# Performance work log

Hardware: AMD Instinct MI355X
Metric: run time of the kernel (lower is better)

## Reference

```python
import jax, jax.numpy as jnp
import numpy as np

D_MODEL = 1024
NUM_HEADS = 16
D_K = D_MODEL // NUM_HEADS


def setup_inputs() -> dict:
    key = jax.random.key(0)
    ks = jax.random.split(key, 7)
    B, S = 4, 2048
    lim = float(np.sqrt(6.0 / (D_MODEL + D_MODEL)))  # xavier uniform
    x = jax.random.normal(ks[0], (B, S, D_MODEL), dtype=jnp.float32)
    w_q = jax.random.uniform(ks[1], (D_MODEL, D_MODEL), jnp.float32, -lim, lim)
    w_k = jax.random.uniform(ks[2], (D_MODEL, D_MODEL), jnp.float32, -lim, lim)
    w_v = jax.random.uniform(ks[3], (D_MODEL, D_MODEL), jnp.float32, -lim, lim)
    w_o = jax.random.uniform(ks[4], (D_MODEL, D_MODEL), jnp.float32, -lim, lim)
    b_o = jnp.zeros((D_MODEL,), jnp.float32)
    ln_g = jnp.ones((D_MODEL,), jnp.float32)
    ln_b = jnp.zeros((D_MODEL,), jnp.float32)
    return {"x": x, "w_q": w_q, "w_k": w_k, "w_v": w_v, "w_o": w_o,
            "b_o": b_o, "ln_g": ln_g, "ln_b": ln_b}


def _layer_norm(y, g, b, eps=1e-5):
    mu = jnp.mean(y, axis=-1, keepdims=True)
    var = jnp.var(y, axis=-1, keepdims=True)
    return (y - mu) * jax.lax.rsqrt(var + eps) * g + b


def reference(x, w_q, w_k, w_v, w_o, b_o, ln_g, ln_b):
    B, S, D = x.shape
    # Linear weights stored torch-style [out, in]: y = x @ W^T
    def proj(w):
        return jnp.einsum('bsd,ed->bse', x, w).reshape(B, S, NUM_HEADS, D_K).transpose(0, 2, 1, 3)
    Q, K, V = proj(w_q), proj(w_k), proj(w_v)  # [B, H, S, d_k]
    scores = jnp.einsum('bhqd,bhkd->bhqk', Q, K) / jnp.sqrt(jnp.float32(D_K))
    attn = jax.nn.softmax(scores, axis=-1)  # dropout identity at eval
    out = jnp.einsum('bhqk,bhkd->bhqd', attn, V)  # [B, H, S, d_k]
    out = out.transpose(0, 2, 1, 3).reshape(B, S, D)
    out = jnp.einsum('bsd,ed->bse', out, w_o) + b_o
    return _layer_norm(x + out, ln_g, ln_b)
```

## Files before the change

kernel.cpp:

```cpp
#include <hip/hip_runtime.h>

typedef __bf16 bf16;
typedef bf16 v8bf __attribute__((ext_vector_type(8)));
typedef bf16 v4bf __attribute__((ext_vector_type(4)));
typedef float v4f __attribute__((ext_vector_type(4)));
typedef float v16f __attribute__((ext_vector_type(16)));
typedef unsigned int u32;
typedef u32 v4u __attribute__((ext_vector_type(4)));

#define GAS __attribute__((address_space(1)))
#define LAS __attribute__((address_space(3)))

constexpr int D    = 1024;
constexpr int ROWS = 8192;

__global__ __launch_bounds__(256) void cast_all(
    const float* __restrict__ x,
    const float* __restrict__ wq, const float* __restrict__ wk,
    const float* __restrict__ wv, const float* __restrict__ wo,
    bf16* __restrict__ xb, bf16* __restrict__ wqb, bf16* __restrict__ wkb,
    bf16* __restrict__ wvb, bf16* __restrict__ wob)
{
    int i = blockIdx.x * 256 + threadIdx.x;
    const float* src; bf16* dst; int off;
    if (i < 2 * 1024 * 1024) { src = x; dst = xb; off = i; }
    else {
        int j = i - 2 * 1024 * 1024;
        int w = j >> 18;
        off = j & ((1 << 18) - 1);
        src = (w == 0) ? wq : (w == 1) ? wk : (w == 2) ? wv : wo;
        dst = (w == 0) ? wqb : (w == 1) ? wkb : (w == 2) ? wvb : wob;
    }
    float4 v = ((const float4*)src)[off];
    v4bf o;
    o[0] = (bf16)v.x; o[1] = (bf16)v.y; o[2] = (bf16)v.z; o[3] = (bf16)v.w;
    ((v4bf*)dst)[off] = o;
}

template<int MODE, int NTN>
__global__ __launch_bounds__(512, 2) void gemm8(
    const bf16* __restrict__ A, const bf16* __restrict__ W,
    bf16* __restrict__ Oq, bf16* __restrict__ Ok, bf16* __restrict__ Ov,
    float* __restrict__ Of, const float* __restrict__ bias,
    const float* __restrict__ X)
{
    __shared__ bf16 Abuf[3][256 * 64];
    __shared__ bf16 Bbuf[3][128 * 64];

    const int id   = blockIdx.x;
    const int wgid = (id & 7) * (4 * NTN) + (id >> 3);
    const int mT   = wgid / NTN;
    const int nT   = wgid - mT * NTN;
    const long rowA0 = (long)mT * 256;
    const long colB0 = (long)nT * 128;

    const int tid  = threadIdx.x;
    const int lane = tid & 63;
    const int wave = tid >> 6;
    const int quad = lane >> 4;
    const int l16  = lane & 15;
    const int wm   = (wave >> 1) * 64;
    const int wn   = (wave & 1) * 64;

    const int srow = wave * 8 + (lane >> 3);
    const int scol = ((lane & 7) ^ (lane >> 3)) * 8;
    const bf16* gA = A + (rowA0 + srow) * D + scol;
    const bf16* gB = W + (colB0 + srow) * D + scol;
    const int dstOff = wave * 512;

    const v4f vzero = {0.f, 0.f, 0.f, 0.f};
    v4f acc[4][4];
    #pragma unroll
    for (int i = 0; i < 4; i++)
        #pragma unroll
        for (int j = 0; j < 4; j++) acc[i][j] = vzero;

    int sa[2], sb[2];
    #pragma unroll
    for (int ks = 0; ks < 2; ks++) {
        const int ch = ((ks * 4 + quad) ^ (l16 & 7)) * 8;
        sa[ks] = (wm + l16) * 64 + ch;
        sb[ks] = (wn + l16) * 64 + ch;
    }

    auto stage_full = [&](int bi, int t) {
        const bf16* a = gA + (long)t * 64;
        const bf16* b = gB + (long)t * 64;
        #pragma unroll
        for (int i = 0; i < 4; i++)
            __builtin_amdgcn_global_load_lds(
                (const GAS void*)(a + (long)i * 64 * D),
                (LAS void*)(&Abuf[bi][i * 4096 + dstOff]), 16, 0, 0);
        #pragma unroll
        for (int i = 0; i < 2; i++)
            __builtin_amdgcn_global_load_lds(
                (const GAS void*)(b + (long)i * 64 * D),
                (LAS void*)(&Bbuf[bi][i * 4096 + dstOff]), 16, 0, 0);
    };

    constexpr int NT = 16;
    stage_full(0, 0);
    stage_full(1, 1);
    asm volatile("s_waitcnt vmcnt(6)" ::: "memory");
    __builtin_amdgcn_s_barrier();

    for (int t = 0; t < NT; ++t) {
        const int bi = t % 3;
        const int bs = (t + 2) % 3;
        const bf16* As = &Abuf[bi][0];
        const bf16* Bs = &Bbuf[bi][0];
        #pragma unroll
        for (int ks = 0; ks < 2; ++ks) {
            v8bf af[4], bf4[4];
            #pragma unroll
            for (int mi = 0; mi < 4; mi++)
                af[mi] = *(const v8bf*)(As + sa[ks] + mi * 1024);
            #pragma unroll
            for (int ni = 0; ni < 4; ni++)
                bf4[ni] = *(const v8bf*)(Bs + sb[ks] + ni * 1024);

            if (t + 2 < NT) {
                const bf16* a2 = gA + (long)(t + 2) * 64;
                const bf16* b2 = gB + (long)(t + 2) * 64;
                if (ks == 0) {
                    __builtin_amdgcn_global_load_lds(
                        (const GAS void*)(a2),
                        (LAS void*)(&Abuf[bs][dstOff]), 16, 0, 0);
                    __builtin_amdgcn_global_load_lds(
                        (const GAS void*)(a2 + (long)64 * D),
                        (LAS void*)(&Abuf[bs][4096 + dstOff]), 16, 0, 0);
                    __builtin_amdgcn_global_load_lds(
                        (const GAS void*)(b2),
                        (LAS void*)(&Bbuf[bs][dstOff]), 16, 0, 0);
                } else {
                    __builtin_amdgcn_global_load_lds(
                        (const GAS void*)(a2 + (long)128 * D),
                        (LAS void*)(&Abuf[bs][2 * 4096 + dstOff]), 16, 0, 0);
                    __builtin_amdgcn_global_load_lds(
                        (const GAS void*)(a2 + (long)192 * D),
                        (LAS void*)(&Abuf[bs][3 * 4096 + dstOff]), 16, 0, 0);
                    __builtin_amdgcn_global_load_lds(
                        (const GAS void*)(b2 + (long)64 * D),
                        (LAS void*)(&Bbuf[bs][4096 + dstOff]), 16, 0, 0);
                }
            }

            if (ks == 1 && t + 1 < NT) {
                if (t + 2 < NT) asm volatile("s_waitcnt vmcnt(6)" ::: "memory");
                else            asm volatile("s_waitcnt vmcnt(0)" ::: "memory");
            }

            __builtin_amdgcn_s_barrier();
            asm volatile("s_waitcnt lgkmcnt(0)" ::: "memory");
            __builtin_amdgcn_sched_barrier(0);
            __builtin_amdgcn_s_setprio(1);
            #pragma unroll
            for (int mi = 0; mi < 4; mi++)
                #pragma unroll
                for (int ni = 0; ni < 4; ni++)
                    acc[mi][ni] = __builtin_amdgcn_mfma_f32_16x16x32_bf16(
                        af[mi], bf4[ni], acc[mi][ni], 0, 0, 0);
            __builtin_amdgcn_s_setprio(0);
            __builtin_amdgcn_s_barrier();
        }
    }

    const float qscale = 0.125f * 1.44269504f;

    if (MODE == 0) {
        const int z = (int)(colB0 >> 10);
        #pragma unroll
        for (int mi = 0; mi < 4; mi++) {
            #pragma unroll
            for (int ni = 0; ni < 4; ni++) {
                const long col = colB0 + wn + ni * 16 + l16;
                const long c   = col & 1023;
                const long row0 = rowA0 + wm + mi * 16 + quad * 4;
                if (z == 2) {
                    const long h_ = c >> 6, dd = c & 63;
                    const long b_ = row0 >> 11, s0 = row0 & 2047;
                    v4bf pk;
                    #pragma unroll
                    for (int r = 0; r < 4; r++) pk[r] = (bf16)acc[mi][ni][r];
                    *(v4bf*)(Ov + ((b_ * 16 + h_) * 64 + dd) * 2048 + s0) = pk;
                } else {
                    bf16* Ob = (z == 0) ? Oq : Ok;
                    #pragma unroll
                    for (int r = 0; r < 4; r++) {
                        float v = acc[mi][ni][r];
                        if (z == 0) v *= qscale;
                        Ob[(row0 + r) * D + c] = (bf16)v;
                    }
                }
            }
        }
    } else {
        #pragma unroll
        for (int mi = 0; mi < 4; mi++) {
            #pragma unroll
            for (int ni = 0; ni < 4; ni++) {
                const long col = colB0 + wn + ni * 16 + l16;
                const float bv = bias[col];
                #pragma unroll
                for (int r = 0; r < 4; r++) {
                    const long row = rowA0 + wm + mi * 16 + quad * 4 + r;
                    Of[row * D + col] = acc[mi][ni][r] + bv + X[row * D + col];
                }
            }
        }
    }
}

__global__ __launch_bounds__(512, 2) void attn_kernel(
    const bf16* __restrict__ Q, const bf16* __restrict__ Kg,
    const bf16* __restrict__ VtG, bf16* __restrict__ O)
{
    const int id  = blockIdx.x;
    const int xcd = id & 7, j = id >> 3;
    const int qt  = j & 7;
    const int g   = xcd + 8 * (j >> 3);
    const int h   = g & 15, b = g >> 4;

    const int tid  = threadIdx.x;
    const int lane = tid & 63;
    const int wave = tid >> 6;
    const int l31  = lane & 31;
    const int hi   = lane >> 5;

    __shared__ bf16 Kt[3][64 * 64];
    __shared__ bf16 Vt[3][64 * 64];

    const long qrow = (long)(b * 2048 + qt * 256 + wave * 32 + l31);
    v8bf qB[4];
    #pragma unroll
    for (int f = 0; f < 4; f++)
        qB[f] = *(const v8bf*)(Q + qrow * D + h * 64 + f * 16 + hi * 8);

    const v16f z16 = {0.f,0.f,0.f,0.f,0.f,0.f,0.f,0.f,
                      0.f,0.f,0.f,0.f,0.f,0.f,0.f,0.f};
    v16f o_acc[2];
    o_acc[0] = z16; o_acc[1] = z16;
    float l0 = 0.f, l1 = 0.f;

    const int iR  = tid >> 3;
    const int c8  = tid & 7;
    const int csw = ((c8 ^ (iR & 7)) * 8);
    const bf16* kSrc = Kg  + (long)b * 2048 * D + h * 64 + csw + (long)iR * D;
    const bf16* vSrc = VtG + (long)(b * 16 + h) * 64 * 2048 + csw + (long)iR * 2048;
    const int ldsOff = wave * 512;

    auto stage = [&](int bi, int t) {
        __builtin_amdgcn_global_load_lds(
            (const GAS void*)(kSrc + (long)t * 64 * D),
            (LAS void*)(&Kt[bi][ldsOff]), 16, 0, 0);
        __builtin_amdgcn_global_load_lds(
            (const GAS void*)(vSrc + t * 64),
            (LAS void*)(&Vt[bi][ldsOff]), 16, 0, 0);
    };

    auto compute = [&](const int bq) {
        #pragma unroll
        for (int ko = 0; ko < 2; ko++) {
            const int krow = ko * 32 + l31;
            const int ksw  = krow & 7;
            v8bf kA[4];
            #pragma unroll
            for (int f = 0; f < 4; f++)
                kA[f] = *(const v8bf*)(&Kt[bq][krow * 64 + (((2 * f + hi) ^ ksw) * 8)]);
            __builtin_amdgcn_s_setprio(1);
            v16f st = __builtin_amdgcn_mfma_f32_32x32x16_bf16(kA[0], qB[0], z16, 0, 0, 0);
            st = __builtin_amdgcn_mfma_f32_32x32x16_bf16(kA[1], qB[1], st, 0, 0, 0);
            st = __builtin_amdgcn_mfma_f32_32x32x16_bf16(kA[2], qB[2], st, 0, 0, 0);
            st = __builtin_amdgcn_mfma_f32_32x32x16_bf16(kA[3], qB[3], st, 0, 0, 0);
            __builtin_amdgcn_s_setprio(0);

            float p[16];
            #pragma unroll
            for (int r = 0; r < 16; r++) {
                p[r] = __builtin_amdgcn_exp2f(st[r]);
                if (r & 1) l1 += p[r]; else l0 += p[r];
            }

            #pragma unroll
            for (int u = 0; u < 2; u++) {
                const int s = ko * 2 + u;
                u32 a0, a1, b0, b1;
                asm("v_cvt_pk_bf16_f32 %0, %1, %2" : "=v"(a0) : "v"(p[u*8+0]), "v"(p[u*8+1]));
                asm("v_cvt_pk_bf16_f32 %0, %1, %2" : "=v"(a1) : "v"(p[u*8+2]), "v"(p[u*8+3]));
                asm("v_cvt_pk_bf16_f32 %0, %1, %2" : "=v"(b0) : "v"(p[u*8+4]), "v"(p[u*8+5]));
                asm("v_cvt_pk_bf16_f32 %0, %1, %2" : "=v"(b1) : "v"(p[u*8+6]), "v"(p[u*8+7]));
                asm("v_permlane32_swap_b32 %0, %1" : "+v"(a0), "+v"(b0));
                asm("v_permlane32_swap_b32 %0, %1" : "+v"(a1), "+v"(b1));
                v4u w; w[0] = a0; w[1] = a1; w[2] = b0; w[3] = b1;
                const v8bf pa = __builtin_bit_cast(v8bf, w);
                const int vsw = (l31 & 7);
                v8bf vb0 = *(const v8bf*)(&Vt[bq][(l31)      * 64 + (((2 * s + hi) ^ vsw) * 8)]);
                v8bf vb1 = *(const v8bf*)(&Vt[bq][(32 + l31) * 64 + (((2 * s + hi) ^ vsw) * 8)]);
                __builtin_amdgcn_s_setprio(1);
                o_acc[0] = __builtin_amdgcn_mfma_f32_32x32x16_bf16(pa, vb0, o_acc[0], 0, 0, 0);
                o_acc[1] = __builtin_amdgcn_mfma_f32_32x32x16_bf16(pa, vb1, o_acc[1], 0, 0, 0);
                __builtin_amdgcn_s_setprio(0);
            }
        }
    };

    stage(0, 0);
    stage(1, 1);
    asm volatile("s_waitcnt vmcnt(2)" ::: "memory");
    __builtin_amdgcn_s_barrier();

    for (int kt = 0; kt < 32; ++kt) {
        const int bi = kt % 3;
        if (kt + 2 < 32) stage((kt + 2) % 3, kt + 2);
        compute(bi);
        if (kt + 1 < 32) {
            if (kt + 2 < 32) asm volatile("s_waitcnt vmcnt(2)" ::: "memory");
            else             asm volatile("s_waitcnt vmcnt(0)" ::: "memory");
            __builtin_amdgcn_s_barrier();
        }
    }

    float l_acc = l0 + l1;
    l_acc += __shfl_xor(l_acc, 32);

    const long obase = (long)(b * 2048 + qt * 256 + wave * 32);
    #pragma unroll
    for (int r = 0; r < 16; r++) {
        const int qp = (r & 3) + 8 * (r >> 2) + 4 * hi;
        const float inv = 1.f / __shfl(l_acc, qp);
        O[(obase + qp) * D + h * 64 + l31]      = (bf16)(o_acc[0][r] * inv);
        O[(obase + qp) * D + h * 64 + 32 + l31] = (bf16)(o_acc[1][r] * inv);
    }
}

__global__ __launch_bounds__(256) void ln_kernel(
    const float* __restrict__ g, const float* __restrict__ beta,
    float* __restrict__ out)
{
    const int row = blockIdx.x;
    const int t = threadIdx.x;
    const int lane = t & 63, wave = t >> 6;
    const long base = (long)row * D + t * 4;

    float4 yv = *(const float4*)(out + base);
    float y0 = yv.x, y1 = yv.y, y2 = yv.z, y3 = yv.w;
    float s1 = y0 + y1 + y2 + y3;
    float s2 = y0*y0 + y1*y1 + y2*y2 + y3*y3;
    #pragma unroll
    for (int off = 1; off < 64; off <<= 1) {
        s1 += __shfl_xor(s1, off);
        s2 += __shfl_xor(s2, off);
    }
    __shared__ float r1[4], r2[4];
    if (lane == 0) { r1[wave] = s1; r2[wave] = s2; }
    __syncthreads();
    float S1 = r1[0] + r1[1] + r1[2] + r1[3];
    float S2 = r2[0] + r2[1] + r2[2] + r2[3];
    float mu  = S1 * (1.f / 1024.f);
    float var = S2 * (1.f / 1024.f) - mu * mu;
    float rsd = rsqrtf(var + 1e-5f);

    float4 gv = *(const float4*)(g + t * 4);
    float4 bv = *(const float4*)(beta + t * 4);
    float4 o;
    o.x = (y0 - mu) * rsd * gv.x + bv.x;
    o.y = (y1 - mu) * rsd * gv.y + bv.y;
    o.z = (y2 - mu) * rsd * gv.z + bv.z;
    o.w = (y3 - mu) * rsd * gv.w + bv.w;
    *(float4*)(out + base) = o;
}

extern "C" void kernel_launch(void* const* d_in, const int* in_sizes, int n_in,
                              void* d_out, int out_size, void* d_ws, size_t ws_size,
                              hipStream_t stream)
{
    const float* x   = (const float*)d_in[0];
    const float* wq  = (const float*)d_in[1];
    const float* wk  = (const float*)d_in[2];
    const float* wv  = (const float*)d_in[3];
    const float* wo  = (const float*)d_in[4];
    const float* bo  = (const float*)d_in[5];
    const float* lng = (const float*)d_in[6];
    const float* lnb = (const float*)d_in[7];
    float* out = (float*)d_out;

    char* ws = (char*)d_ws;
    bf16* xb  = (bf16*)(ws);
    bf16* wqb = (bf16*)(ws + (size_t)16 * 1024 * 1024);
    bf16* wkb = wqb + 1024 * 1024;
    bf16* wvb = wkb + 1024 * 1024;
    bf16* wob = wvb + 1024 * 1024;
    bf16* Qb  = (bf16*)(ws + (size_t)24 * 1024 * 1024);
    bf16* Kb  = Qb + (size_t)ROWS * D;
    bf16* VtG = Kb + (size_t)ROWS * D;
    bf16* Ab  = VtG + (size_t)ROWS * D;

    cast_all<<<12288, 256, 0, stream>>>(x, wq, wk, wv, wo,
                                        xb, wqb, wkb, wvb, wob);

    gemm8<0, 24><<<768, 512, 0, stream>>>(xb, wqb, Qb, Kb, VtG,
                                          nullptr, nullptr, nullptr);

    attn_kernel<<<dim3(512, 1, 1), 512, 0, stream>>>(Qb, Kb, VtG, Ab);

    gemm8<1, 8><<<256, 512, 0, stream>>>(Ab, wob, nullptr, nullptr, nullptr,
                                         out, bo, x);

    ln_kernel<<<8192, 256, 0, stream>>>(lng, lnb, out);
}
```

Baseline: 278.2 us.

## Double query rows per wave in attention, deepen K/V pipeline, MFMA row sums

Each attention block now handles 512 query rows, with each wave owning two 32-row query tiles, so every K/V tile staged in LDS is reused across twice as many queries. The grid is halved to 256 blocks. The LDS ring grows to six slots and is consumed two tiles per barrier, which halves the number of barriers. Softmax row sums now come from an extra MFMA against a ones vector instead of scalar adds and shuffles. The costs are more registers and LDS per block, lower occupancy, and fewer blocks than the 256 CUs can absorb evenly.

Result: no change. 279.1 us (+0.3%).

```diff
diff --git a/kernel.cpp b/kernel.cpp
--- a/kernel.cpp
+++ b/kernel.cpp
@@ -217,8 +217,8 @@
 {
     const int id  = blockIdx.x;
     const int xcd = id & 7, j = id >> 3;
-    const int qt  = j & 7;
-    const int g   = xcd + 8 * (j >> 3);
+    const int qt  = j & 3;
+    const int g   = xcd + 8 * (j >> 2);
     const int h   = g & 15, b = g >> 4;
 
     const int tid  = threadIdx.x;
@@ -227,20 +227,30 @@
     const int l31  = lane & 31;
     const int hi   = lane >> 5;
 
-    __shared__ bf16 Kt[3][64 * 64];
-    __shared__ bf16 Vt[3][64 * 64];
-
-    const long qrow = (long)(b * 2048 + qt * 256 + wave * 32 + l31);
-    v8bf qB[4];
-    #pragma unroll
-    for (int f = 0; f < 4; f++)
-        qB[f] = *(const v8bf*)(Q + qrow * D + h * 64 + f * 16 + hi * 8);
+    __shared__ bf16 Kt[6][64 * 64];
+    __shared__ bf16 Vt[6][64 * 64];
+
+    v8bf qB[2][4];
+    #pragma unroll
+    for (int qh = 0; qh < 2; qh++) {
+        const long qrow = (long)(b * 2048 + qt * 512 + wave * 64 + qh * 32 + l31);
+        #pragma unroll
+        for (int f = 0; f < 4; f++)
+            qB[qh][f] = *(const v8bf*)(Q + qrow * D + h * 64 + f * 16 + hi * 8);
+    }
 
     const v16f z16 = {0.f,0.f,0.f,0.f,0.f,0.f,0.f,0.f,
                       0.f,0.f,0.f,0.f,0.f,0.f,0.f,0.f};
-    v16f o_acc[2];
-    o_acc[0] = z16; o_acc[1] = z16;
-    float l0 = 0.f, l1 = 0.f;
+    v16f o_acc[2][2], o_l[2];
+    #pragma unroll
+    for (int qh = 0; qh < 2; qh++) {
+        o_acc[qh][0] = z16; o_acc[qh][1] = z16; o_l[qh] = z16;
+    }
+
+    const bf16 one = (bf16)1.0f;
+    v8bf ones;
+    #pragma unroll
+    for (int i = 0; i < 8; i++) ones[i] = one;
 
     const int iR  = tid >> 3;
     const int c8  = tid & 7;
@@ -249,16 +259,16 @@
     const bf16* vSrc = VtG + (long)(b * 16 + h) * 64 * 2048 + csw + (long)iR * 2048;
     const int ldsOff = wave * 512;
 
-    auto stage = [&](int bi, int t) {
+    auto stage = [&](int slot, int t) {
         __builtin_amdgcn_global_load_lds(
             (const GAS void*)(kSrc + (long)t * 64 * D),
-            (LAS void*)(&Kt[bi][ldsOff]), 16, 0, 0);
+            (LAS void*)(&Kt[slot][ldsOff]), 16, 0, 0);
         __builtin_amdgcn_global_load_lds(
             (const GAS void*)(vSrc + t * 64),
-            (LAS void*)(&Vt[bi][ldsOff]), 16, 0, 0);
+            (LAS void*)(&Vt[slot][ldsOff]), 16, 0, 0);
     };
 
-    auto compute = [&](const int bq) {
+    auto compute = [&](const bf16* kb, const bf16* vb) {
         #pragma unroll
         for (int ko = 0; ko < 2; ko++) {
             const int krow = ko * 32 + l31;
@@ -266,70 +276,93 @@
             v8bf kA[4];
             #pragma unroll
             for (int f = 0; f < 4; f++)
-                kA[f] = *(const v8bf*)(&Kt[bq][krow * 64 + (((2 * f + hi) ^ ksw) * 8)]);
+                kA[f] = *(const v8bf*)(kb + krow * 64 + (((2 * f + hi) ^ ksw) * 8));
             __builtin_amdgcn_s_setprio(1);
-            v16f st = __builtin_amdgcn_mfma_f32_32x32x16_bf16(kA[0], qB[0], z16, 0, 0, 0);
-            st = __builtin_amdgcn_mfma_f32_32x32x16_bf16(kA[1], qB[1], st, 0, 0, 0);
-            st = __builtin_amdgcn_mfma_f32_32x32x16_bf16(kA[2], qB[2], st, 0, 0, 0);
-            st = __builtin_amdgcn_mfma_f32_32x32x16_bf16(kA[3], qB[3], st, 0, 0, 0);
+            v16f st0 = __builtin_amdgcn_mfma_f32_32x32x16_bf16(kA[0], qB[0][0], z16, 0, 0, 0);
+            v16f st1 = __builtin_amdgcn_mfma_f32_32x32x16_bf16(kA[0], qB[1][0], z16, 0, 0, 0);
+            #pragma unroll
+            for (int f = 1; f < 4; f++) {
+                st0 = __builtin_amdgcn_mfma_f32_32x32x16_bf16(kA[f], qB[0][f], st0, 0, 0, 0);
+                st1 = __builtin_amdgcn_mfma_f32_32x32x16_bf16(kA[f], qB[1][f], st1, 0, 0, 0);
+            }
             __builtin_amdgcn_s_setprio(0);
 
-            float p[16];
+            float p0[16], p1[16];
             #pragma unroll
             for (int r = 0; r < 16; r++) {
-                p[r] = __builtin_amdgcn_exp2f(st[r]);
-                if (r & 1) l1 += p[r]; else l0 += p[r];
+                p0[r] = __builtin_amdgcn_exp2f(st0[r]);
+                p1[r] = __builtin_amdgcn_exp2f(st1[r]);
             }
 
             #pragma unroll
             for (int u = 0; u < 2; u++) {
                 const int s = ko * 2 + u;
-                u32 a0, a1, b0, b1;
-                asm("v_cvt_pk_bf16_f32 %0, %1, %2" : "=v"(a0) : "v"(p[u*8+0]), "v"(p[u*8+1]));
-                asm("v_cvt_pk_bf16_f32 %0, %1, %2" : "=v"(a1) : "v"(p[u*8+2]), "v"(p[u*8+3]));
-                asm("v_cvt_pk_bf16_f32 %0, %1, %2" : "=v"(b0) : "v"(p[u*8+4]), "v"(p[u*8+5]));
-                asm("v_cvt_pk_bf16_f32 %0, %1, %2" : "=v"(b1) : "v"(p[u*8+6]), "v"(p[u*8+7]));
+                u32 a0, a1, b0, b1, c0, c1, d0, d1;
+                asm("v_cvt_pk_bf16_f32 %0, %1, %2" : "=v"(a0) : "v"(p0[u*8+0]), "v"(p0[u*8+1]));
+                asm("v_cvt_pk_bf16_f32 %0, %1, %2" : "=v"(a1) : "v"(p0[u*8+2]), "v"(p0[u*8+3]));
+                asm("v_cvt_pk_bf16_f32 %0, %1, %2" : "=v"(b0) : "v"(p0[u*8+4]), "v"(p0[u*8+5]));
+                asm("v_cvt_pk_bf16_f32 %0, %1, %2" : "=v"(b1) : "v"(p0[u*8+6]), "v"(p0[u*8+7]));
                 asm("v_permlane32_swap_b32 %0, %1" : "+v"(a0), "+v"(b0));
                 asm("v_permlane32_swap_b32 %0, %1" : "+v"(a1), "+v"(b1));
-                v4u w; w[0] = a0; w[1] = a1; w[2] = b0; w[3] = b1;
-                const v8bf pa = __builtin_bit_cast(v8bf, w);
+                asm("v_cvt_pk_bf16_f32 %0, %1, %2" : "=v"(c0) : "v"(p1[u*8+0]), "v"(p1[u*8+1]));
+                asm("v_cvt_pk_bf16_f32 %0, %1, %2" : "=v"(c1) : "v"(p1[u*8+2]), "v"(p1[u*8+3]));
+                asm("v_cvt_pk_bf16_f32 %0, %1, %2" : "=v"(d0) : "v"(p1[u*8+4]), "v"(p1[u*8+5]));
+                asm("v_cvt_pk_bf16_f32 %0, %1, %2" : "=v"(d1) : "v"(p1[u*8+6]), "v"(p1[u*8+7]));
+                asm("v_permlane32_swap_b32 %0, %1" : "+v"(c0), "+v"(d0));
+                asm("v_permlane32_swap_b32 %0, %1" : "+v"(c1), "+v"(d1));
+                v4u w0; w0[0] = a0; w0[1] = a1; w0[2] = b0; w0[3] = b1;
+                v4u w1; w1[0] = c0; w1[1] = c1; w1[2] = d0; w1[3] = d1;
+                const v8bf pa0 = __builtin_bit_cast(v8bf, w0);
+                const v8bf pa1 = __builtin_bit_cast(v8bf, w1);
                 const int vsw = (l31 & 7);
-                v8bf vb0 = *(const v8bf*)(&Vt[bq][(l31)      * 64 + (((2 * s + hi) ^ vsw) * 8)]);
-                v8bf vb1 = *(const v8bf*)(&Vt[bq][(32 + l31) * 64 + (((2 * s + hi) ^ vsw) * 8)]);
+                v8bf vb0 = *(const v8bf*)(vb + (l31)      * 64 + (((2 * s + hi) ^ vsw) * 8));
+                v8bf vb1 = *(const v8bf*)(vb + (32 + l31) * 64 + (((2 * s + hi) ^ vsw) * 8));
                 __builtin_amdgcn_s_setprio(1);
-                o_acc[0] = __builtin_amdgcn_mfma_f32_32x32x16_bf16(pa, vb0, o_acc[0], 0, 0, 0);
-                o_acc[1] = __builtin_amdgcn_mfma_f32_32x32x16_bf16(pa, vb1, o_acc[1], 0, 0, 0);
+                o_acc[0][0] = __builtin_amdgcn_mfma_f32_32x32x16_bf16(pa0, vb0, o_acc[0][0], 0, 0, 0);
+                o_acc[0][1] = __builtin_amdgcn_mfma_f32_32x32x16_bf16(pa0, vb1, o_acc[0][1], 0, 0, 0);
+                o_acc[1][0] = __builtin_amdgcn_mfma_f32_32x32x16_bf16(pa1, vb0, o_acc[1][0], 0, 0, 0);
+                o_acc[1][1] = __builtin_amdgcn_mfma_f32_32x32x16_bf16(pa1, vb1, o_acc[1][1], 0, 0, 0);
+                o_l[0] = __builtin_amdgcn_mfma_f32_32x32x16_bf16(pa0, ones, o_l[0], 0, 0, 0);
+                o_l[1] = __builtin_amdgcn_mfma_f32_32x32x16_bf16(pa1, ones, o_l[1], 0, 0, 0);
                 __builtin_amdgcn_s_setprio(0);
             }
         }
     };
 
-    stage(0, 0);
-    stage(1, 1);
-    asm volatile("s_waitcnt vmcnt(2)" ::: "memory");
+    stage(0, 0); stage(1, 1); stage(2, 2); stage(3, 3);
+    asm volatile("s_waitcnt vmcnt(4)" ::: "memory");
     __builtin_amdgcn_s_barrier();
 
-    for (int kt = 0; kt < 32; ++kt) {
-        const int bi = kt % 3;
-        if (kt + 2 < 32) stage((kt + 2) % 3, kt + 2);
-        compute(bi);
-        if (kt + 1 < 32) {
-            if (kt + 2 < 32) asm volatile("s_waitcnt vmcnt(2)" ::: "memory");
-            else             asm volatile("s_waitcnt vmcnt(0)" ::: "memory");
+    int sA = 0;
+    for (int p = 0; p < 16; ++p) {
+        const int t4 = 2 * p + 4;
+        if (t4 < 32) {
+            int ss0 = sA + 4; if (ss0 >= 6) ss0 -= 6;
+            int ss1 = sA + 5; if (ss1 >= 6) ss1 -= 6;
+            stage(ss0, t4);
+            stage(ss1, t4 + 1);
+        }
+        compute(&Kt[sA][0], &Vt[sA][0]);
+        compute(&Kt[sA + 1][0], &Vt[sA + 1][0]);
+        if (p < 15) {
+            if (p < 14) asm volatile("s_waitcnt vmcnt(4)" ::: "memory");
+            else        asm volatile("s_waitcnt vmcnt(0)" ::: "memory");
             __builtin_amdgcn_s_barrier();
         }
-    }
-
-    float l_acc = l0 + l1;
-    l_acc += __shfl_xor(l_acc, 32);
-
-    const long obase = (long)(b * 2048 + qt * 256 + wave * 32);
-    #pragma unroll
-    for (int r = 0; r < 16; r++) {
-        const int qp = (r & 3) + 8 * (r >> 2) + 4 * hi;
-        const float inv = 1.f / __shfl(l_acc, qp);
-        O[(obase + qp) * D + h * 64 + l31]      = (bf16)(o_acc[0][r] * inv);
-        O[(obase + qp) * D + h * 64 + 32 + l31] = (bf16)(o_acc[1][r] * inv);
+        sA += 2; if (sA >= 6) sA -= 6;
+    }
+
+    const long obase = (long)(b * 2048 + qt * 512 + wave * 64);
+    #pragma unroll
+    for (int qh = 0; qh < 2; qh++) {
+        #pragma unroll
+        for (int r = 0; r < 16; r++) {
+            const int qp = (r & 3) + 8 * (r >> 2) + 4 * hi;
+            const float inv = 1.f / o_l[qh][r];
+            const long row = obase + qh * 32 + qp;
+            O[row * D + h * 64 + l31]      = (bf16)(o_acc[qh][0][r] * inv);
+            O[row * D + h * 64 + 32 + l31] = (bf16)(o_acc[qh][1][r] * inv);
+        }
     }
 }
 
@@ -401,7 +434,7 @@
     gemm8<0, 24><<<768, 512, 0, stream>>>(xb, wqb, Qb, Kb, VtG,
                                           nullptr, nullptr, nullptr);
 
-    attn_kernel<<<dim3(512, 1, 1), 512, 0, stream>>>(Qb, Kb, VtG, Ab);
+    attn_kernel<<<dim3(256, 1, 1), 512, 0, stream>>>(Qb, Kb, VtG, Ab);
 
     gemm8<1, 8><<<256, 512, 0, stream>>>(Ab, wob, nullptr, nullptr, nullptr,
                                          out, bo, x);
```
